# Performance work log

Measured on AMD Instinct MI355X. Metric: run time of the kernel, lower is better.

## Reference

```python
import jax, jax.numpy as jnp
import numpy as np

N = 100000
E = 1600000
IN_FT = 128
OUT_FT = 128
SELF_LOOP_FILL = 3.0


def setup_inputs() -> dict:
    key = jax.random.key(0)
    k1, k2, k3, k4 = jax.random.split(key, 4)
    seq = jax.random.normal(k1, (N, IN_FT), dtype=jnp.float32)
    edge_index = jax.random.randint(k2, (2, E), 0, N, dtype=jnp.int64)
    edge_weight = jax.random.uniform(k3, (E,), dtype=jnp.float32)
    # xavier_uniform for Linear(in_ft, out_ft): W shape [out_ft, in_ft]
    limit = float(np.sqrt(6.0 / (IN_FT + OUT_FT)))
    W = jax.random.uniform(k4, (OUT_FT, IN_FT), dtype=jnp.float32, minval=-limit, maxval=limit)
    return {"seq": seq, "edge_weight": edge_weight, "W": W, "edge_index": edge_index}


def reference(seq, edge_weight, W, edge_index):
    n = seq.shape[0]
    # dropout with drop_prob=0.0 is identity; fc_1: x = seq @ W^T
    x = seq @ W.T  # [N, out_ft]
    # add self loops with fill_value=3.0
    loops = jnp.arange(n, dtype=edge_index.dtype)
    row = jnp.concatenate([edge_index[0], loops])
    col = jnp.concatenate([edge_index[1], loops])
    w = jnp.concatenate([edge_weight, jnp.full((n,), SELF_LOOP_FILL, dtype=edge_weight.dtype)])
    # symmetric normalization: deg^-1/2 [row] * w * deg^-1/2 [col]
    deg = jax.ops.segment_sum(w, row, num_segments=n)
    deg_inv_sqrt = jnp.where(deg > 0, jax.lax.rsqrt(deg), jnp.zeros_like(deg))
    norm = deg_inv_sqrt[row] * w * deg_inv_sqrt[col]
    # sparse aggregation: out[r] += norm_e * x[c]
    out = jax.ops.segment_sum(norm[:, None] * x[col], row, num_segments=n)
    return jax.nn.relu(out)
```

## Files before the change

kernel.cpp:

```cpp
#include <hip/hip_runtime.h>


#define TPB 256
#define NBROWS 256
#define BCAP 4608
#define RCAP 48
#define EPB 2048
#define GPW 4

typedef __attribute__((ext_vector_type(8))) short s16x8;
typedef __attribute__((ext_vector_type(4))) float f32x4;

__global__ void k_init(int* __restrict__ cursor, int m) {
    int i = blockIdx.x * TPB + threadIdx.x;
    if (i < m) cursor[i] = 0;
}

__global__ __launch_bounds__(TPB) void k_partition(const int* __restrict__ ei,
                                                   const float* __restrict__ ew,
                                                   int* __restrict__ cursor,
                                                   int2* __restrict__ part,
                                                   int e, int nb) {
    __shared__ int hist[512];
    __shared__ int chunk[512];
    int t = threadIdx.x;
    hist[t] = 0; hist[t + 256] = 0;
    chunk[t] = 0; chunk[t + 256] = 0;
    __syncthreads();

    long base = (long)blockIdx.x * EPB;
    for (int j = 0; j < EPB / 256; ++j) {
        long idx = base + j * 256 + t;
        if (idx < e) atomicAdd(&hist[ei[idx] >> 8], 1);
    }
    __syncthreads();
    for (int b = t; b < nb; b += TPB) {
        int h = hist[b];
        chunk[b] = (h > 0) ? atomicAdd(&cursor[b * 16], h) : 0;
    }
    __syncthreads();
    hist[t] = 0; hist[t + 256] = 0;
    __syncthreads();
    for (int j = 0; j < EPB / 256; ++j) {
        long idx = base + j * 256 + t;
        if (idx < e) {
            int r = ei[idx];
            int c = ei[e + idx];
            float w = ew[idx];
            int b = r >> 8;
            int rank = atomicAdd(&hist[b], 1);
            int dst = chunk[b] + rank;
            if (dst < BCAP)
                part[(long)b * BCAP + dst] =
                    make_int2(((r & 255) << 17) | c, __float_as_int(w));
        }
    }
}

__global__ __launch_bounds__(TPB) void k_build(const int2* __restrict__ part,
                                               const int* __restrict__ cursor,
                                               unsigned* __restrict__ slotsG,
                                               float2* __restrict__ dc,
                                               float* __restrict__ dis, int n) {
    __shared__ unsigned lslot[NBROWS * RCAP];
    __shared__ int rowcnt[NBROWS];
    int b = blockIdx.x, t = threadIdx.x;
    rowcnt[t] = 0;
    for (int j = t; j < NBROWS * RCAP; j += TPB) lslot[j] = 0;
    __syncthreads();

    int m = cursor[b * 16]; if (m > BCAP) m = BCAP;
    for (int i = t; i < m; i += TPB) {
        int2 en = part[(long)b * BCAP + i];
        int rl = ((unsigned)en.x) >> 17;
        int c  = en.x & 0x1FFFF;
        float w = __int_as_float(en.y);
        int pos = atomicAdd(&rowcnt[rl], 1);
        if (pos < RCAP) {
            int q = (int)(w * 32768.0f);
            if (q > 32767) q = 32767;
            lslot[rl * RCAP + pos] = ((unsigned)q << 17) | (unsigned)c;
        }
    }
    __syncthreads();

    int node = b * NBROWS + t;
    if (node < n) {
        int rc = rowcnt[t]; if (rc > RCAP) rc = RCAP;
        float s = 0.0f;
        for (int k = 0; k < rc; ++k)
            s += ((float)(lslot[t * RCAP + k] >> 17) + 0.5f) * (1.0f / 32768.0f);
        float di = rsqrtf(3.0f + s);
        dis[node] = di;
        dc[node] = make_float2(di, __int_as_float(rc));
    }
    for (int j = t; j < NBROWS * RCAP; j += TPB)
        slotsG[(long)b * (NBROWS * RCAP) + j] = lslot[j];
}

__device__ inline unsigned bf16rne(float x) {
    unsigned u = __float_as_uint(x);
    u += 0x7FFF + ((u >> 16) & 1);
    return u >> 16;
}

__global__ __launch_bounds__(TPB) void k_prescale(const float* __restrict__ seq,
                                                  const float* __restrict__ dis,
                                                  unsigned* __restrict__ xb, long npairs) {
    long p = (long)blockIdx.x * TPB + threadIdx.x;
    if (p >= npairs) return;
    float d = dis[p >> 6];
    float2 s = ((const float2*)seq)[p];
    xb[p] = bf16rne(d * s.x) | (bf16rne(d * s.y) << 16);
}

__global__ __launch_bounds__(TPB) void k_gather(const unsigned* __restrict__ xb,
                                                const unsigned* __restrict__ slotsG,
                                                const float2* __restrict__ dc,
                                                float* __restrict__ y, int n) {
    int wave = threadIdx.x >> 6, lane = threadIdx.x & 63;
    int node0 = blockIdx.x * (4 * GPW) + wave * GPW;
    if (node0 >= n) return;

    float di[GPW];
    int   m[GPW];
    int   cl[GPW];
    float vl[GPW];
    float2 acc[GPW];
    int mmax = 0;

#pragma unroll
    for (int q = 0; q < GPW; ++q) {
        int node = node0 + q;
        bool has = (node < n);
        float2 d = has ? dc[node] : make_float2(0.0f, __int_as_float(0));
        di[q] = d.x;
        m[q] = __float_as_int(d.y);
        if (m[q] > mmax) mmax = m[q];
        unsigned s = (has && lane < m[q]) ? slotsG[(long)node * RCAP + lane] : 0u;
        int c = (int)(s & 0x1FFFF); if (c > n - 1) c = n - 1;
        cl[q] = c;
        vl[q] = (lane < m[q]) ? ((float)(s >> 17) + 0.5f) * (1.0f / 32768.0f) : 0.0f;
        unsigned u = has ? xb[(long)node * 64 + lane] : 0u;
        acc[q].x = 3.0f * __uint_as_float(u << 16);
        acc[q].y = 3.0f * __uint_as_float(u & 0xFFFF0000u);
    }

    unsigned xva[GPW], xvb[GPW];
    float    va[GPW],  vb[GPW];

#pragma unroll
    for (int q = 0; q < GPW; ++q) {
        int c = __shfl(cl[q], 0);
        va[q] = __shfl(vl[q], 0);
        xva[q] = xb[(long)c * 64 + lane];
    }

    for (int p = 0; p < mmax; p += 2) {
#pragma unroll
        for (int q = 0; q < GPW; ++q) {
            int c = __shfl(cl[q], p + 1);
            vb[q] = __shfl(vl[q], p + 1);
            xvb[q] = xb[(long)c * 64 + lane];
        }
#pragma unroll
        for (int q = 0; q < GPW; ++q) {
            acc[q].x = fmaf(va[q], __uint_as_float(xva[q] << 16), acc[q].x);
            acc[q].y = fmaf(va[q], __uint_as_float(xva[q] & 0xFFFF0000u), acc[q].y);
        }
        if (p + 2 < mmax) {
#pragma unroll
            for (int q = 0; q < GPW; ++q) {
                int c = __shfl(cl[q], p + 2);
                va[q] = __shfl(vl[q], p + 2);
                xva[q] = xb[(long)c * 64 + lane];
            }
        }
#pragma unroll
        for (int q = 0; q < GPW; ++q) {
            acc[q].x = fmaf(vb[q], __uint_as_float(xvb[q] << 16), acc[q].x);
            acc[q].y = fmaf(vb[q], __uint_as_float(xvb[q] & 0xFFFF0000u), acc[q].y);
        }
    }

#pragma unroll
    for (int q = 0; q < GPW; ++q) {
        int node = node0 + q;
        if (node < n)
            ((float2*)(y + (long)node * 128))[lane] =
                make_float2(di[q] * acc[q].x, di[q] * acc[q].y);
    }
}

__global__ __launch_bounds__(TPB) void k_gemm(float* __restrict__ y,
                                              const float* __restrict__ W, int n) {
    __shared__ short wlds[128 * 128];
    __shared__ short ylds[128 * 128];
    int t = threadIdx.x;
    long base = (long)blockIdx.x * 128;

#pragma unroll
    for (int i = 0; i < 8; ++i) {
        int G = i * 256 + t;
        int j = G >> 4, g = G & 15;
        const float* src = W + j * 128 + g * 8;
        float4 f0 = *(const float4*)src;
        float4 f1 = *(const float4*)(src + 4);
        union { s16x8 s; uint4 u; } pk;
        pk.u.x = bf16rne(f0.x) | (bf16rne(f0.y) << 16);
        pk.u.y = bf16rne(f0.z) | (bf16rne(f0.w) << 16);
        pk.u.z = bf16rne(f1.x) | (bf16rne(f1.y) << 16);
        pk.u.w = bf16rne(f1.z) | (bf16rne(f1.w) << 16);
        *(s16x8*)&wlds[j * 128 + ((g ^ (j & 15)) << 3)] = pk.s;
    }
#pragma unroll
    for (int i = 0; i < 8; ++i) {
        int G = i * 256 + t;
        int r = G >> 4, g = G & 15;
        long gr = base + r; if (gr >= n) gr = n - 1;
        const float* src = y + gr * 128 + g * 8;
        float4 f0 = *(const float4*)src;
        float4 f1 = *(const float4*)(src + 4);
        union { s16x8 s; uint4 u; } pk;
        pk.u.x = bf16rne(f0.x) | (bf16rne(f0.y) << 16);
        pk.u.y = bf16rne(f0.z) | (bf16rne(f0.w) << 16);
        pk.u.z = bf16rne(f1.x) | (bf16rne(f1.y) << 16);
        pk.u.w = bf16rne(f1.z) | (bf16rne(f1.w) << 16);
        *(s16x8*)&ylds[r * 128 + ((g ^ (r & 15)) << 3)] = pk.s;
    }
    __syncthreads();

    int wave = t >> 6, lane = t & 63;
    int quad = lane >> 4, l15 = lane & 15;

    f32x4 acc[2][8];
#pragma unroll
    for (int h = 0; h < 2; ++h)
#pragma unroll
        for (int ct = 0; ct < 8; ++ct)
            acc[h][ct] = (f32x4){0.0f, 0.0f, 0.0f, 0.0f};

    int r0 = wave * 32 + l15;
    int r1 = wave * 32 + 16 + l15;

#pragma unroll
    for (int kc = 0; kc < 4; ++kc) {
        int gA = kc * 4 + quad;
        s16x8 a0 = *(const s16x8*)&ylds[r0 * 128 + ((gA ^ l15) << 3)];
        s16x8 a1 = *(const s16x8*)&ylds[r1 * 128 + ((gA ^ l15) << 3)];
#pragma unroll
        for (int ct = 0; ct < 8; ++ct) {
            int j = ct * 16 + l15;
            s16x8 b = *(const s16x8*)&wlds[j * 128 + ((gA ^ l15) << 3)];
            acc[0][ct] = __builtin_amdgcn_mfma_f32_16x16x32_bf16(a0, b, acc[0][ct], 0, 0, 0);
            acc[1][ct] = __builtin_amdgcn_mfma_f32_16x16x32_bf16(a1, b, acc[1][ct], 0, 0, 0);
        }
    }

#pragma unroll
    for (int h = 0; h < 2; ++h) {
        long rloc = wave * 32 + h * 16 + quad * 4;
#pragma unroll
        for (int i = 0; i < 4; ++i) {
            long gr = base + rloc + i;
            if (gr < n) {
                float* dst = y + gr * 128 + l15;
#pragma unroll
                for (int ct = 0; ct < 8; ++ct)
                    dst[ct * 16] = fmaxf(acc[h][ct][i], 0.0f);
            }
        }
    }
}

extern "C" void kernel_launch(void* const* d_in, const int* in_sizes, int n_in,
                              void* d_out, int out_size, void* d_ws, size_t ws_size,
                              hipStream_t stream) {
    const float* seq = (const float*)d_in[0];
    const float* ew  = (const float*)d_in[1];
    const float* W   = (const float*)d_in[2];
    const int*   ei  = (const int*)d_in[3];
    float* out = (float*)d_out;

    int n = in_sizes[0] / 128;
    int e = in_sizes[1];
    int nb = (n + NBROWS - 1) / NBROWS;

    char* w8 = (char*)d_ws;
    unsigned* xb   = (unsigned*)w8;
    size_t off = (size_t)n * 64 * 4;
    int2* part     = (int2*)(w8 + off);
    off += (size_t)nb * BCAP * 8;
    unsigned* slotsG = (unsigned*)(w8 + off);
    off += (size_t)nb * NBROWS * RCAP * 4;
    int* cursor    = (int*)(w8 + off);
    off += (size_t)nb * 16 * 4;
    float2* dc     = (float2*)(w8 + off);
    off += (size_t)n * 8;
    float* dis     = (float*)(w8 + off);

    long npairs = (long)n * 64;

    k_init     <<<(nb * 16 + TPB - 1) / TPB, TPB, 0, stream>>>(cursor, nb * 16);
    k_partition<<<(e + EPB - 1) / EPB, TPB, 0, stream>>>(ei, ew, cursor, part, e, nb);
    k_build    <<<nb, TPB, 0, stream>>>(part, cursor, slotsG, dc, dis, n);
    k_prescale <<<(int)((npairs + TPB - 1) / TPB), TPB, 0, stream>>>(seq, dis, xb, npairs);
    k_gather   <<<(n + 4 * GPW - 1) / (4 * GPW), TPB, 0, stream>>>(xb, slotsG, dc, out, n);
    k_gemm     <<<(n + 127) / 128, TPB, 0, stream>>>(out, W, n);
}
```

Baseline: 271.3 us.

## Fuse gather aggregation with bf16 MFMA GEMM epilogue per 16-node block

Merges the gather kernel and the GEMM kernel into one. Each block aggregates 16 nodes, packs the results to bf16 in shared memory and multiplies them by W with MFMA, then applies ReLU and writes the output. This removes the fp32 write and re-read of the intermediate aggregated matrix plus one launch. In exchange, every small block now converts the whole 128x128 W to bf16 in LDS, and the 32KB+ of shared memory per block may limit occupancy of the latency-bound gather.

```diff
diff --git a/kernel.cpp b/kernel.cpp
--- a/kernel.cpp
+++ b/kernel.cpp
@@ -114,13 +114,32 @@
     xb[p] = bf16rne(d * s.x) | (bf16rne(d * s.y) << 16);
 }
 
-__global__ __launch_bounds__(TPB) void k_gather(const unsigned* __restrict__ xb,
-                                                const unsigned* __restrict__ slotsG,
-                                                const float2* __restrict__ dc,
-                                                float* __restrict__ y, int n) {
-    int wave = threadIdx.x >> 6, lane = threadIdx.x & 63;
+__global__ __launch_bounds__(TPB) void k_gather_gemm(const unsigned* __restrict__ xb,
+                                                     const unsigned* __restrict__ slotsG,
+                                                     const float2* __restrict__ dc,
+                                                     const float* __restrict__ W,
+                                                     float* __restrict__ out, int n) {
+    __shared__ short wlds[128 * 128];
+    __shared__ short ylds[16 * 128];
+    int t = threadIdx.x;
+    int wave = t >> 6, lane = t & 63;
+
+#pragma unroll
+    for (int i = 0; i < 8; ++i) {
+        int G = i * 256 + t;
+        int j = G >> 4, g = G & 15;
+        const float* src = W + j * 128 + g * 8;
+        float4 f0 = *(const float4*)src;
+        float4 f1 = *(const float4*)(src + 4);
+        union { s16x8 s; uint4 u; } pk;
+        pk.u.x = bf16rne(f0.x) | (bf16rne(f0.y) << 16);
+        pk.u.y = bf16rne(f0.z) | (bf16rne(f0.w) << 16);
+        pk.u.z = bf16rne(f1.x) | (bf16rne(f1.y) << 16);
+        pk.u.w = bf16rne(f1.z) | (bf16rne(f1.w) << 16);
+        *(s16x8*)&wlds[j * 128 + ((g ^ (j & 15)) << 3)] = pk.s;
+    }
+
     int node0 = blockIdx.x * (4 * GPW) + wave * GPW;
-    if (node0 >= n) return;
 
     float di[GPW];
     int   m[GPW];
@@ -185,90 +204,38 @@
 
 #pragma unroll
     for (int q = 0; q < GPW; ++q) {
-        int node = node0 + q;
-        if (node < n)
-            ((float2*)(y + (long)node * 128))[lane] =
-                make_float2(di[q] * acc[q].x, di[q] * acc[q].y);
-    }
-}
-
-__global__ __launch_bounds__(TPB) void k_gemm(float* __restrict__ y,
-                                              const float* __restrict__ W, int n) {
-    __shared__ short wlds[128 * 128];
-    __shared__ short ylds[128 * 128];
-    int t = threadIdx.x;
-    long base = (long)blockIdx.x * 128;
-
-#pragma unroll
-    for (int i = 0; i < 8; ++i) {
-        int G = i * 256 + t;
-        int j = G >> 4, g = G & 15;
-        const float* src = W + j * 128 + g * 8;
-        float4 f0 = *(const float4*)src;
-        float4 f1 = *(const float4*)(src + 4);
-        union { s16x8 s; uint4 u; } pk;
-        pk.u.x = bf16rne(f0.x) | (bf16rne(f0.y) << 16);
-        pk.u.y = bf16rne(f0.z) | (bf16rne(f0.w) << 16);
-        pk.u.z = bf16rne(f1.x) | (bf16rne(f1.y) << 16);
-        pk.u.w = bf16rne(f1.z) | (bf16rne(f1.w) << 16);
-        *(s16x8*)&wlds[j * 128 + ((g ^ (j & 15)) << 3)] = pk.s;
-    }
-#pragma unroll
-    for (int i = 0; i < 8; ++i) {
-        int G = i * 256 + t;
-        int r = G >> 4, g = G & 15;
-        long gr = base + r; if (gr >= n) gr = n - 1;
-        const float* src = y + gr * 128 + g * 8;
-        float4 f0 = *(const float4*)src;
-        float4 f1 = *(const float4*)(src + 4);
-        union { s16x8 s; uint4 u; } pk;
-        pk.u.x = bf16rne(f0.x) | (bf16rne(f0.y) << 16);
-        pk.u.y = bf16rne(f0.z) | (bf16rne(f0.w) << 16);
-        pk.u.z = bf16rne(f1.x) | (bf16rne(f1.y) << 16);
-        pk.u.w = bf16rne(f1.z) | (bf16rne(f1.w) << 16);
-        *(s16x8*)&ylds[r * 128 + ((g ^ (r & 15)) << 3)] = pk.s;
-    }
-    __syncthreads();
-
-    int wave = t >> 6, lane = t & 63;
+        int r = wave * GPW + q;
+        unsigned pkv = bf16rne(di[q] * acc[q].x) | (bf16rne(di[q] * acc[q].y) << 16);
+        ((unsigned*)ylds)[r * 64 + ((((lane >> 2) ^ r) & 15) << 2) + (lane & 3)] = pkv;
+    }
+    __syncthreads();
+
     int quad = lane >> 4, l15 = lane & 15;
-
-    f32x4 acc[2][8];
-#pragma unroll
-    for (int h = 0; h < 2; ++h)
-#pragma unroll
-        for (int ct = 0; ct < 8; ++ct)
-            acc[h][ct] = (f32x4){0.0f, 0.0f, 0.0f, 0.0f};
-
-    int r0 = wave * 32 + l15;
-    int r1 = wave * 32 + 16 + l15;
+    f32x4 acc2[2];
+    acc2[0] = (f32x4){0.0f, 0.0f, 0.0f, 0.0f};
+    acc2[1] = (f32x4){0.0f, 0.0f, 0.0f, 0.0f};
 
 #pragma unroll
     for (int kc = 0; kc < 4; ++kc) {
         int gA = kc * 4 + quad;
-        s16x8 a0 = *(const s16x8*)&ylds[r0 * 128 + ((gA ^ l15) << 3)];
-        s16x8 a1 = *(const s16x8*)&ylds[r1 * 128 + ((gA ^ l15) << 3)];
-#pragma unroll
-        for (int ct = 0; ct < 8; ++ct) {
-            int j = ct * 16 + l15;
+        s16x8 a = *(const s16x8*)&ylds[l15 * 128 + ((gA ^ l15) << 3)];
+#pragma unroll
+        for (int h = 0; h < 2; ++h) {
+            int j = (wave * 2 + h) * 16 + l15;
             s16x8 b = *(const s16x8*)&wlds[j * 128 + ((gA ^ l15) << 3)];
-            acc[0][ct] = __builtin_amdgcn_mfma_f32_16x16x32_bf16(a0, b, acc[0][ct], 0, 0, 0);
-            acc[1][ct] = __builtin_amdgcn_mfma_f32_16x16x32_bf16(a1, b, acc[1][ct], 0, 0, 0);
-        }
-    }
-
+            acc2[h] = __builtin_amdgcn_mfma_f32_16x16x32_bf16(a, b, acc2[h], 0, 0, 0);
+        }
+    }
+
+    long base = (long)blockIdx.x * 16;
 #pragma unroll
     for (int h = 0; h < 2; ++h) {
-        long rloc = wave * 32 + h * 16 + quad * 4;
+        int ct = wave * 2 + h;
 #pragma unroll
         for (int i = 0; i < 4; ++i) {
-            long gr = base + rloc + i;
-            if (gr < n) {
-                float* dst = y + gr * 128 + l15;
-#pragma unroll
-                for (int ct = 0; ct < 8; ++ct)
-                    dst[ct * 16] = fmaxf(acc[h][ct][i], 0.0f);
-            }
+            long gr = base + quad * 4 + i;
+            if (gr < n)
+                out[gr * 128 + ct * 16 + l15] = fmaxf(acc2[h][i], 0.0f);
         }
     }
 }
@@ -301,10 +268,9 @@
 
     long npairs = (long)n * 64;
 
-    k_init     <<<(nb * 16 + TPB - 1) / TPB, TPB, 0, stream>>>(cursor, nb * 16);
-    k_partition<<<(e + EPB - 1) / EPB, TPB, 0, stream>>>(ei, ew, cursor, part, e, nb);
-    k_build    <<<nb, TPB, 0, stream>>>(part, cursor, slotsG, dc, dis, n);
-    k_prescale <<<(int)((npairs + TPB - 1) / TPB), TPB, 0, stream>>>(seq, dis, xb, npairs);
-    k_gather   <<<(n + 4 * GPW - 1) / (4 * GPW), TPB, 0, stream>>>(xb, slotsG, dc, out, n);
-    k_gemm     <<<(n + 127) / 128, TPB, 0, stream>>>(out, W, n);
-}
+    k_init       <<<(nb * 16 + TPB - 1) / TPB, TPB, 0, stream>>>(cursor, nb * 16);
+    k_partition  <<<(e + EPB - 1) / EPB, TPB, 0, stream>>>(ei, ew, cursor, part, e, nb);
+    k_build      <<<nb, TPB, 0, stream>>>(part, cursor, slotsG, dc, dis, n);
+    k_prescale   <<<(int)((npairs + TPB - 1) / TPB), TPB, 0, stream>>>(seq, dis, xb, npairs);
+    k_gather_gemm<<<(n + 4 * GPW - 1) / (4 * GPW), TPB, 0, stream>>>(xb, slotsG, dc, W, out, n);
+}
```

After: 270.9 us. No clear change (-0.2%).
